# Performance work log

Hardware: AMD Instinct MI355X
Metric: run time of the kernel (lower is better)

## Reference

```python
import jax, jax.numpy as jnp
import numpy as np

N_NODES = 50000
N_EDGES = 800000
D_FEAT = 64


def setup_inputs() -> dict:
    key = jax.random.key(0)
    k_x, k_e, k_w = jax.random.split(key, 3)
    x = jax.random.normal(k_x, (N_NODES, D_FEAT), dtype=jnp.float32)
    edge_index = jax.random.randint(k_e, (2, N_EDGES), 0, N_NODES, dtype=jnp.int64)
    # message MLP params (phi_Theta): single linear + ReLU
    W = jax.random.normal(k_w, (D_FEAT, D_FEAT), dtype=jnp.float32) / np.sqrt(D_FEAT)
    b = jnp.zeros((D_FEAT,), dtype=jnp.float32)
    return {"x": x, "edge_index": edge_index, "W": W, "b": b}


def reference(x, edge_index, W, b):
    # flow = source_to_target: messages flow from edge_index[0] (j) to edge_index[1] (i)
    src = edge_index[0]  # j: source nodes (gather)
    dst = edge_index[1]  # i: target nodes (scatter index)
    n_nodes = x.shape[0]
    # __collect__: index_select gather of source node features -> x_j [E, D]
    x_j = x[src]
    # message: per-edge MLP  phi(x_j) = relu(x_j W + b)
    msg = jax.nn.relu(jnp.einsum('ed,df->ef', x_j, W) + b)
    # aggregate: scatter-add into target nodes (aggr='add', dim_size = size_i)
    out = jax.ops.segment_sum(msg, dst, num_segments=n_nodes)
    # update: identity
    return out
```

## Files before the change

kernel.cpp:

```cpp
#include <hip/hip_runtime.h>
#include <hip/hip_bf16.h>

#define D 64
#define CAP 64

__device__ __forceinline__ float bf2f(unsigned short u) {
    return __uint_as_float((unsigned int)u << 16);
}
__device__ __forceinline__ unsigned short f2bf(float f) {
    unsigned int u = __float_as_uint(f);
    unsigned int r = (u + 0x7fffu + ((u >> 16) & 1u)) >> 16;
    return (unsigned short)r;
}

__global__ __launch_bounds__(256) void node_mlp_kernel(
    const float* __restrict__ x, const float* __restrict__ W,
    const float* __restrict__ b, unsigned short* __restrict__ m,
    int* __restrict__ cnt, int n_nodes) {
    for (int i = blockIdx.x * blockDim.x + threadIdx.x; i < n_nodes;
         i += gridDim.x * blockDim.x) cnt[i] = 0;

    const int lane = threadIdx.x & 63;
    float w[D];
    #pragma unroll
    for (int k = 0; k < D; ++k) w[k] = W[k * D + lane];
    const float bias = b[lane];

    const int wave = (blockIdx.x * blockDim.x + threadIdx.x) >> 6;
    const int nwaves = (gridDim.x * blockDim.x) >> 6;

    for (int row = wave; row < n_nodes; row += nwaves) {
        const float4* xr = (const float4*)(x + (size_t)row * D);
        float acc = bias;
        #pragma unroll
        for (int kk = 0; kk < D / 4; ++kk) {
            float4 xv = xr[kk];
            acc = fmaf(xv.x, w[4 * kk + 0], acc);
            acc = fmaf(xv.y, w[4 * kk + 1], acc);
            acc = fmaf(xv.z, w[4 * kk + 2], acc);
            acc = fmaf(xv.w, w[4 * kk + 3], acc);
        }
        m[(size_t)row * D + lane] = f2bf(fmaxf(acc, 0.0f));
    }
}

__global__ __launch_bounds__(256) void append_kernel(
    const int* __restrict__ src, const int* __restrict__ dst,
    int* __restrict__ cnt, unsigned short* __restrict__ slots, int n_edges) {
    int e = blockIdx.x * 256 + threadIdx.x;
    if (e >= n_edges) return;
    int d = dst[e];
    int s = src[e];
    int pos = atomicAdd(&cnt[d], 1);
    if (pos < CAP) slots[(size_t)d * CAP + pos] = (unsigned short)s;
}

__global__ __launch_bounds__(256) void gather_accum_kernel(
    const unsigned short* __restrict__ slots, const int* __restrict__ cnt,
    const unsigned short* __restrict__ m, float* __restrict__ out, int n_nodes) {
    int node = blockIdx.x * 4 + (threadIdx.x >> 6);
    if (node >= n_nodes) return;
    int lane = threadIdx.x & 63;

    int c = min(cnt[node], CAP);
    unsigned int idx = (lane < c) ? (unsigned int)slots[(size_t)node * CAP + lane] : 0u;

    float acc = 0.0f;
    int k = 0;
    for (; k + 4 <= c; k += 4) {
        unsigned int s0 = __shfl(idx, k + 0);
        unsigned int s1 = __shfl(idx, k + 1);
        unsigned int s2 = __shfl(idx, k + 2);
        unsigned int s3 = __shfl(idx, k + 3);
        float v0 = bf2f(m[(size_t)s0 * D + lane]);
        float v1 = bf2f(m[(size_t)s1 * D + lane]);
        float v2 = bf2f(m[(size_t)s2 * D + lane]);
        float v3 = bf2f(m[(size_t)s3 * D + lane]);
        acc += (v0 + v1) + (v2 + v3);
    }
    for (; k < c; ++k) {
        unsigned int s = __shfl(idx, k);
        acc += bf2f(m[(size_t)s * D + lane]);
    }
    out[(size_t)node * D + lane] = acc;
}

__global__ __launch_bounds__(256) void edge_scatter_kernel(
    const int* __restrict__ src, const int* __restrict__ dst,
    const unsigned short* __restrict__ m, float* __restrict__ out, int n_edges) {
    long long t = (long long)blockIdx.x * blockDim.x + threadIdx.x;
    int e = (int)(t >> 4);
    if (e >= n_edges) return;
    int c = (int)(t & 15) << 2;
    int s = src[e];
    int d = dst[e];
    const ushort4 v = *(const ushort4*)(m + (size_t)s * D + c);
    float* o = out + (size_t)d * D + c;
    atomicAdd(o + 0, bf2f(v.x));
    atomicAdd(o + 1, bf2f(v.y));
    atomicAdd(o + 2, bf2f(v.z));
    atomicAdd(o + 3, bf2f(v.w));
}

static inline size_t align_up(size_t v, size_t a) { return (v + a - 1) & ~(a - 1); }

extern "C" void kernel_launch(void* const* d_in, const int* in_sizes, int n_in,
                              void* d_out, int out_size, void* d_ws, size_t ws_size,
                              hipStream_t stream) {
    const float* x = (const float*)d_in[0];
    const int* edge_index = (const int*)d_in[1];
    const float* W = (const float*)d_in[2];
    const float* b = (const float*)d_in[3];
    float* out = (float*)d_out;

    const int n_nodes = in_sizes[0] / D;
    const int n_edges = in_sizes[1] / 2;
    const int* src = edge_index;
    const int* dst = edge_index + n_edges;

    size_t off = 0;
    unsigned short* m = (unsigned short*)((char*)d_ws + off);
    off = align_up(off + (size_t)n_nodes * D * sizeof(unsigned short), 256);
    int* cnt = (int*)((char*)d_ws + off);
    off = align_up(off + (size_t)n_nodes * sizeof(int), 256);
    unsigned short* slots = (unsigned short*)((char*)d_ws + off);
    off = align_up(off + (size_t)n_nodes * CAP * sizeof(unsigned short), 256);
    const size_t needed = off;

    node_mlp_kernel<<<512, 256, 0, stream>>>(x, W, b, m, cnt, n_nodes);

    if (ws_size >= needed && n_nodes <= 65536) {
        int eblocks = (n_edges + 255) / 256;
        append_kernel<<<eblocks, 256, 0, stream>>>(src, dst, cnt, slots, n_edges);
        gather_accum_kernel<<<(n_nodes + 3) / 4, 256, 0, stream>>>(
            slots, cnt, m, out, n_nodes);
    } else {
        hipMemsetAsync(d_out, 0, (size_t)out_size * sizeof(float), stream);
        long long total_threads = (long long)n_edges * 16;
        int scat_blocks = (int)((total_threads + 255) / 256);
        edge_scatter_kernel<<<scat_blocks, 256, 0, stream>>>(src, dst, m, out, n_edges);
    }
}
```

Before: 167.6 us.

## Fuse node MLP and edge append into one heterogeneous kernel launch

```diff
diff --git a/kernel.cpp b/kernel.cpp
--- a/kernel.cpp
+++ b/kernel.cpp
@@ -3,6 +3,7 @@
 
 #define D 64
 #define CAP 64
+#define EUNROLL 4
 
 __device__ __forceinline__ float bf2f(unsigned short u) {
     return __uint_as_float((unsigned int)u << 16);
@@ -13,46 +14,55 @@
     return (unsigned short)r;
 }
 
-__global__ __launch_bounds__(256) void node_mlp_kernel(
+__global__ __launch_bounds__(256) void fused_mlp_append_kernel(
     const float* __restrict__ x, const float* __restrict__ W,
     const float* __restrict__ b, unsigned short* __restrict__ m,
-    int* __restrict__ cnt, int n_nodes) {
-    for (int i = blockIdx.x * blockDim.x + threadIdx.x; i < n_nodes;
-         i += gridDim.x * blockDim.x) cnt[i] = 0;
+    const int* __restrict__ src, const int* __restrict__ dst,
+    int* __restrict__ cnt, unsigned short* __restrict__ slots,
+    int n_nodes, int n_edges, int mlp_blocks) {
+    if ((int)blockIdx.x < mlp_blocks) {
+        const int lane = threadIdx.x & 63;
+        float w[D];
+        #pragma unroll
+        for (int k = 0; k < D; ++k) w[k] = W[k * D + lane];
+        const float bias = b[lane];
 
-    const int lane = threadIdx.x & 63;
-    float w[D];
-    #pragma unroll
-    for (int k = 0; k < D; ++k) w[k] = W[k * D + lane];
-    const float bias = b[lane];
+        const int wave = (blockIdx.x * 256 + threadIdx.x) >> 6;
+        const int nwaves = (mlp_blocks * 256) >> 6;
 
-    const int wave = (blockIdx.x * blockDim.x + threadIdx.x) >> 6;
-    const int nwaves = (gridDim.x * blockDim.x) >> 6;
-
-    for (int row = wave; row < n_nodes; row += nwaves) {
-        const float4* xr = (const float4*)(x + (size_t)row * D);
-        float acc = bias;
+        for (int row = wave; row < n_nodes; row += nwaves) {
+            const float4* xr = (const float4*)(x + (size_t)row * D);
+            float acc = bias;
+            #pragma unroll
+            for (int kk = 0; kk < D / 4; ++kk) {
+                float4 xv = xr[kk];
+                acc = fmaf(xv.x, w[4 * kk + 0], acc);
+                acc = fmaf(xv.y, w[4 * kk + 1], acc);
+                acc = fmaf(xv.z, w[4 * kk + 2], acc);
+                acc = fmaf(xv.w, w[4 * kk + 3], acc);
+            }
+            m[(size_t)row * D + lane] = f2bf(fmaxf(acc, 0.0f));
+        }
+    } else {
+        const int ablk = blockIdx.x - mlp_blocks;
+        const int base = ablk * 256 * EUNROLL + threadIdx.x;
+        int s[EUNROLL], d[EUNROLL], pos[EUNROLL];
+        bool ok[EUNROLL];
         #pragma unroll
-        for (int kk = 0; kk < D / 4; ++kk) {
-            float4 xv = xr[kk];
-            acc = fmaf(xv.x, w[4 * kk + 0], acc);
-            acc = fmaf(xv.y, w[4 * kk + 1], acc);
-            acc = fmaf(xv.z, w[4 * kk + 2], acc);
-            acc = fmaf(xv.w, w[4 * kk + 3], acc);
+        for (int i = 0; i < EUNROLL; ++i) {
+            int e = base + i * 256;
+            ok[i] = (e < n_edges);
+            s[i] = ok[i] ? src[e] : 0;
+            d[i] = ok[i] ? dst[e] : 0;
         }
-        m[(size_t)row * D + lane] = f2bf(fmaxf(acc, 0.0f));
+        #pragma unroll
+        for (int i = 0; i < EUNROLL; ++i)
+            pos[i] = ok[i] ? atomicAdd(&cnt[d[i]], 1) : CAP;
+        #pragma unroll
+        for (int i = 0; i < EUNROLL; ++i)
+            if (ok[i] && pos[i] < CAP)
+                slots[(size_t)d[i] * CAP + pos[i]] = (unsigned short)s[i];
     }
-}
-
-__global__ __launch_bounds__(256) void append_kernel(
-    const int* __restrict__ src, const int* __restrict__ dst,
-    int* __restrict__ cnt, unsigned short* __restrict__ slots, int n_edges) {
-    int e = blockIdx.x * 256 + threadIdx.x;
-    if (e >= n_edges) return;
-    int d = dst[e];
-    int s = src[e];
-    int pos = atomicAdd(&cnt[d], 1);
-    if (pos < CAP) slots[(size_t)d * CAP + pos] = (unsigned short)s;
 }
 
 __global__ __launch_bounds__(256) void gather_accum_kernel(
@@ -67,22 +77,55 @@
 
     float acc = 0.0f;
     int k = 0;
-    for (; k + 4 <= c; k += 4) {
+    for (; k + 8 <= c; k += 8) {
         unsigned int s0 = __shfl(idx, k + 0);
         unsigned int s1 = __shfl(idx, k + 1);
         unsigned int s2 = __shfl(idx, k + 2);
         unsigned int s3 = __shfl(idx, k + 3);
+        unsigned int s4 = __shfl(idx, k + 4);
+        unsigned int s5 = __shfl(idx, k + 5);
+        unsigned int s6 = __shfl(idx, k + 6);
+        unsigned int s7 = __shfl(idx, k + 7);
         float v0 = bf2f(m[(size_t)s0 * D + lane]);
         float v1 = bf2f(m[(size_t)s1 * D + lane]);
         float v2 = bf2f(m[(size_t)s2 * D + lane]);
         float v3 = bf2f(m[(size_t)s3 * D + lane]);
-        acc += (v0 + v1) + (v2 + v3);
+        float v4 = bf2f(m[(size_t)s4 * D + lane]);
+        float v5 = bf2f(m[(size_t)s5 * D + lane]);
+        float v6 = bf2f(m[(size_t)s6 * D + lane]);
+        float v7 = bf2f(m[(size_t)s7 * D + lane]);
+        acc += ((v0 + v1) + (v2 + v3)) + ((v4 + v5) + (v6 + v7));
     }
     for (; k < c; ++k) {
         unsigned int s = __shfl(idx, k);
         acc += bf2f(m[(size_t)s * D + lane]);
     }
     out[(size_t)node * D + lane] = acc;
+}
+
+__global__ __launch_bounds__(256) void node_mlp_kernel(
+    const float* __restrict__ x, const float* __restrict__ W,
+    const float* __restrict__ b, unsigned short* __restrict__ m, int n_nodes) {
+    const int lane = threadIdx.x & 63;
+    float w[D];
+    #pragma unroll
+    for (int k = 0; k < D; ++k) w[k] = W[k * D + lane];
+    const float bias = b[lane];
+    const int wave = (blockIdx.x * blockDim.x + threadIdx.x) >> 6;
+    const int nwaves = (gridDim.x * blockDim.x) >> 6;
+    for (int row = wave; row < n_nodes; row += nwaves) {
+        const float4* xr = (const float4*)(x + (size_t)row * D);
+        float acc = bias;
+        #pragma unroll
+        for (int kk = 0; kk < D / 4; ++kk) {
+            float4 xv = xr[kk];
+            acc = fmaf(xv.x, w[4 * kk + 0], acc);
+            acc = fmaf(xv.y, w[4 * kk + 1], acc);
+            acc = fmaf(xv.z, w[4 * kk + 2], acc);
+            acc = fmaf(xv.w, w[4 * kk + 3], acc);
+        }
+        m[(size_t)row * D + lane] = f2bf(fmaxf(acc, 0.0f));
+    }
 }
 
 __global__ __launch_bounds__(256) void edge_scatter_kernel(
@@ -127,14 +170,16 @@
     off = align_up(off + (size_t)n_nodes * CAP * sizeof(unsigned short), 256);
     const size_t needed = off;
 
-    node_mlp_kernel<<<512, 256, 0, stream>>>(x, W, b, m, cnt, n_nodes);
-
     if (ws_size >= needed && n_nodes <= 65536) {
-        int eblocks = (n_edges + 255) / 256;
-        append_kernel<<<eblocks, 256, 0, stream>>>(src, dst, cnt, slots, n_edges);
+        hipMemsetAsync(cnt, 0, (size_t)n_nodes * sizeof(int), stream);
+        const int mlp_blocks = 512;
+        const int ablocks = (n_edges + 256 * EUNROLL - 1) / (256 * EUNROLL);
+        fused_mlp_append_kernel<<<mlp_blocks + ablocks, 256, 0, stream>>>(
+            x, W, b, m, src, dst, cnt, slots, n_nodes, n_edges, mlp_blocks);
         gather_accum_kernel<<<(n_nodes + 3) / 4, 256, 0, stream>>>(
             slots, cnt, m, out, n_nodes);
     } else {
+        node_mlp_kernel<<<512, 256, 0, stream>>>(x, W, b, m, n_nodes);
         hipMemsetAsync(d_out, 0, (size_t)out_size * sizeof(float), stream);
         long long total_threads = (long long)n_edges * 16;
         int scat_blocks = (int)((total_threads + 255) / 256);
```

Result: slower. 179.2 us (+6.9%).
